# Kernel optimization log

Hardware: AMD Instinct MI355X
Metric: run time of the kernel (lower is better)

Reference implementation:

```python
import jax, jax.numpy as jnp
import numpy as np


def _gru_step(h, x, Wih, Whh, bih, bhh):
    # PyTorch GRU gate order: reset, update, new
    H = h.shape[-1]
    gx = x @ Wih.T + bih            # [B, 3H]
    gh = h @ Whh.T + bhh            # [B, 3H]
    r = jax.nn.sigmoid(gx[:, :H] + gh[:, :H])
    z = jax.nn.sigmoid(gx[:, H:2 * H] + gh[:, H:2 * H])
    n = jnp.tanh(gx[:, 2 * H:] + r * gh[:, 2 * H:])
    return (1.0 - z) * n + z * h


def setup_inputs() -> dict:
    key = jax.random.key(0)
    ks = jax.random.split(key, 20)
    B, S, L = 32, 200, 50
    Vt, Vs = 50000, 30000
    De, Ds, H = 256, 256, 512
    s = 0.05
    f = jnp.float32
    return {
        "method_code": jax.random.randint(ks[0], (B, S), 0, Vt),
        "method_summary": jax.random.randint(ks[1], (B, L), 0, Vs),
        "use_teacher": 1,
        "enc_emb": jax.random.normal(ks[2], (Vt, De), f) * s,
        "enc_Wih": jax.random.normal(ks[3], (3 * H, De), f) * s,
        "enc_Whh": jax.random.normal(ks[4], (3 * H, H), f) * s,
        "enc_bih": jax.random.normal(ks[5], (3 * H,), f) * s,
        "enc_bhh": jax.random.normal(ks[6], (3 * H,), f) * s,
        "dec_emb": jax.random.normal(ks[7], (Vs, Ds), f) * s,
        "dec_Wih": jax.random.normal(ks[8], (3 * H, Ds), f) * s,
        "dec_Whh": jax.random.normal(ks[9], (3 * H, H), f) * s,
        "dec_bih": jax.random.normal(ks[10], (3 * H,), f) * s,
        "dec_bhh": jax.random.normal(ks[11], (3 * H,), f) * s,
        "W1": jax.random.normal(ks[12], (H, 2 * H), f) * s,
        "b1": jax.random.normal(ks[13], (H,), f) * s,
        "W2": jax.random.normal(ks[14], (Vs, H), f) * s,
        "b2": jax.random.normal(ks[15], (Vs,), f) * s,
    }


def reference(method_code, method_summary, use_teacher,
              enc_emb, enc_Wih, enc_Whh, enc_bih, enc_bhh,
              dec_emb, dec_Wih, dec_Whh, dec_bih, dec_bhh,
              W1, b1, W2, b2):
    B = method_code.shape[0]
    H = enc_Whh.shape[1]
    # ---- GRU encoder over code tokens (hidden=None -> zeros) ----
    x_emb = enc_emb[method_code]                       # [B, S, De]
    h0 = jnp.zeros((B, H), x_emb.dtype)

    def enc_step(h, x):
        h = _gru_step(h, x, enc_Wih, enc_Whh, enc_bih, enc_bhh)
        return h, h

    h_last, enc_seq = jax.lax.scan(enc_step, h0, jnp.swapaxes(x_emb, 0, 1))
    enc_out = jnp.swapaxes(enc_seq, 0, 1)              # [B, S, H]

    # ---- attentive GRU decoder, teacher forcing (use_teacher=True) ----
    tokens = method_summary[:, :-1].T                  # [L-1, B]

    def dec_step(h, tok):
        emb = dec_emb[tok]                             # [B, Ds]
        h = _gru_step(h, emb, dec_Wih, dec_Whh, dec_bih, dec_bhh)
        attn = jax.nn.softmax(jnp.einsum('bh,bsh->bs', h, enc_out), axis=-1)
        ctx = jnp.einsum('bs,bsh->bh', attn, enc_out)  # [B, H]
        c = jnp.concatenate([ctx, h], axis=-1)         # [B, 2H]
        out = jax.nn.relu(c @ W1.T + b1) @ W2.T + b2   # [B, Vs]
        return h, out

    _, outs = jax.lax.scan(dec_step, h_last, tokens)   # [L-1, B, Vs]
    return jnp.swapaxes(outs, 0, 1)                    # [B, L-1, Vs]
```

## Files before the change

kernel.cpp:

```cpp
#include <hip/hip_runtime.h>
#include <cmath>

#define WGS  256
#define NWGR 256
#define DOMS 8
#define JGN  32
#define HBDW 2560
#define TDG  4

typedef float    f32x4 __attribute__((ext_vector_type(4)));
typedef unsigned u32x4 __attribute__((ext_vector_type(4)));
typedef short    s16x8 __attribute__((ext_vector_type(8)));
typedef unsigned short u16x4 __attribute__((ext_vector_type(4)));

#define B_   32
#define S_   200
#define L_   50
#define H_   512
#define DE_  256
#define VS_  30000
#define TD_  49
#define G3_  1536

#define OFF_ENC_OUT ((size_t)(S_*B_*G3_) + (size_t)(TD_*B_*G3_))
#define SZ_ENC_OUT  ((size_t)B_*S_*H_)
#define OFF_HBUF    (OFF_ENC_OUT + SZ_ENC_OUT)
#define SZ_HBUF     ((size_t)DOMS*2*HBDW)
#define OFF_CMAT    (OFF_HBUF + SZ_HBUF)
#define SZ_CMAT     ((size_t)TD_*B_*2*H_)
#define OFF_OUT1    (OFF_CMAT + SZ_CMAT)
#define SZ_OUT1     ((size_t)TD_*B_*H_)
#define OFF_W2HI    ((size_t)0)
#define OFF_W2LO    ((size_t)(VS_*H_/2))
#define OFF_O1HI    (OFF_OUT1 + SZ_OUT1)
#define OFF_O1LO    (OFF_O1HI + (size_t)(TD_*B_*H_/2))

#define RSTR 548
#define KBLK 68

__device__ __forceinline__ u32x4 load_u4_cc(const unsigned* p) {
  u32x4 v;
  asm volatile("global_load_dwordx4 %0, %1, off sc0 sc1" : "=v"(v) : "v"(p) : "memory");
  return v;
}

__device__ __forceinline__ float dot4(f32x4 a, f32x4 b) {
  return a.x * b.x + a.y * b.y + a.z * b.z + a.w * b.w;
}

__device__ __forceinline__ unsigned short f2bf(float f) {
  unsigned u = __float_as_uint(f);
  return (unsigned short)((u + 0x7fffu + ((u >> 16) & 1u)) >> 16);
}
__device__ __forceinline__ float bf2f(unsigned short h) {
  return __uint_as_float(((unsigned)h) << 16);
}

__global__ __launch_bounds__(WGS)
void recurrence_kernel(const int* __restrict__ mc, const int* __restrict__ ms,
                       const float* __restrict__ enc_emb,
                       const float* __restrict__ eWih, const float* __restrict__ eBih,
                       const float* __restrict__ dec_emb,
                       const float* __restrict__ dWih, const float* __restrict__ dBih,
                       const float* __restrict__ eWhh, const float* __restrict__ eBhh,
                       const float* __restrict__ dWhh, const float* __restrict__ dBhh,
                       float* __restrict__ enc_out,
                       float* __restrict__ hbuf,
                       float* __restrict__ Cmat)
{
  __shared__ float hlds[4 * RSTR];
  __shared__ float xlds[4 * 256];
  __shared__ float red[768];
  __shared__ float red2[768];

  const int t   = threadIdx.x;
  const int w   = blockIdx.x;
  const int dom = w >> 5;
  const int jg  = w & (JGN - 1);
  const int kh  = t >> 4;
  const int j   = (jg << 4) + (t & 15);
  const int bt_ = t >> 4;
  const int b_g = (dom << 2) + bt_;
  const int xb  = t >> 6, xc = t & 63;
  const int xb_g = (dom << 2) + xb;

  float* hdom = hbuf + (size_t)dom * (2 * HBDW);

  int rr[3], kb[3];
  #pragma unroll
  for (int i = 0; i < 3; ++i) {
    int g = i * 1024 + (t << 2);
    int blk = g / 80;
    rr[i] = g - blk * 80;
    kb[i] = blk << 4;
  }

  f32x4 whh[3][8];
  auto load_whh = [&](const float* __restrict__ W) {
    #pragma unroll
    for (int g = 0; g < 3; ++g)
      #pragma unroll
      for (int c = 0; c < 8; ++c)
        whh[g][c] = *(const f32x4*)(W + (size_t)(g * H_ + j) * H_ + (kh << 5) + (c << 2));
  };
  f32x4 wih[3][4];
  auto load_wih = [&](const float* __restrict__ W) {
    #pragma unroll
    for (int g = 0; g < 3; ++g)
      #pragma unroll
      for (int c = 0; c < 4; ++c)
        wih[g][c] = *(const f32x4*)(W + (size_t)(g * H_ + j) * DE_ + (kh << 4) + (c << 2));
  };
  load_whh(eWhh);
  load_wih(eWih);

  float bhr = 0.f, bhz = 0.f, bhn = 0.f, bxr = 0.f, bxz = 0.f, bxn = 0.f;
  if (t < 64) {
    bhr = eBhh[j]; bhz = eBhh[H_ + j]; bhn = eBhh[2 * H_ + j];
    bxr = eBih[j]; bxz = eBih[H_ + j]; bxn = eBih[2 * H_ + j];
  }

  auto stage_x = [&](int s) {
    const bool enc = (s < S_);
    int tok = enc ? mc[xb_g * S_ + s] : ms[xb_g * L_ + (s - S_)];
    const float* emb = enc ? enc_emb : dec_emb;
    f32x4 xv = *(const f32x4*)(emb + (size_t)tok * DE_ + (xc << 2));
    *(f32x4*)&xlds[xb * 256 + (xc << 2)] = xv;
  };

  auto compute_acx = [&]() {
    float acx[3][4];
    #pragma unroll
    for (int g = 0; g < 3; ++g)
      #pragma unroll
      for (int b = 0; b < 4; ++b) acx[g][b] = 0.f;
    #pragma unroll
    for (int b = 0; b < 4; ++b) {
      const float* xp = &xlds[b * 256 + (kh << 4)];
      #pragma unroll
      for (int c = 0; c < 4; ++c) {
        f32x4 xv = *(const f32x4*)(xp + (c << 2));
        acx[0][b] += dot4(wih[0][c], xv);
        acx[1][b] += dot4(wih[1][c], xv);
        acx[2][b] += dot4(wih[2][c], xv);
      }
    }
    #pragma unroll
    for (int g = 0; g < 3; ++g)
      #pragma unroll
      for (int b = 0; b < 4; ++b) {
        float u = acx[g][b];
        u += __shfl_xor(u, 16); u += __shfl_xor(u, 32);
        acx[g][b] = u;
      }
    if ((t & 48) == 0) {
      const int base = (t >> 6) * 192 + (t & 15) * 12;
      #pragma unroll
      for (int g = 0; g < 3; ++g)
        #pragma unroll
        for (int b = 0; b < 4; ++b)
          red2[base + g * 4 + b] = acx[g][b];
    }
  };

  stage_x(0);
  __syncthreads();
  compute_acx();

  for (int s = 0; s < S_ + TD_; ++s) {
    const bool enc = (s < S_);

    {
      const unsigned* hb = (const unsigned*)(hdom + (size_t)(s & 1) * HBDW);
      const unsigned tagreq = (unsigned)s;
      u32x4 v0, v1, v2;
      while (true) {
        v0 = load_u4_cc(hb + 0 * 1024 + (t << 2));
        v1 = load_u4_cc(hb + 1 * 1024 + (t << 2));
        if (t < 128) v2 = load_u4_cc(hb + 2 * 1024 + (t << 2));
        asm volatile("s_waitcnt vmcnt(0)" ::: "memory");
        bool ok = true;
        if ((rr[0] & 15) == 0) ok &= ((unsigned)v0.x >= tagreq);
        if ((rr[1] & 15) == 0) ok &= ((unsigned)v1.x >= tagreq);
        if (t < 128 && (rr[2] & 15) == 0) ok &= ((unsigned)v2.x >= tagreq);
        if (__all(ok)) break;
        __builtin_amdgcn_s_sleep(1);
      }
      #define SCAT(vv, ii) { \
        _Pragma("unroll") \
        for (int d = 0; d < 4; ++d) { \
          int pos = rr[ii] + d; \
          if ((pos & 15) != 0) { \
            int p = pos - 1 - (pos >> 4); \
            if (p < 64) { \
              int bb = p >> 4, k = kb[ii] + (p & 15); \
              hlds[bb * RSTR + ((k >> 6) * KBLK) + (k & 63)] = __uint_as_float(vv[d]); \
            } } } }
      SCAT(v0, 0) SCAT(v1, 1)
      if (t < 128) { SCAT(v2, 2) }
      #undef SCAT
    }
    __syncthreads();

    {
      float acc[3][4];
      #pragma unroll
      for (int g = 0; g < 3; ++g)
        #pragma unroll
        for (int b = 0; b < 4; ++b) acc[g][b] = 0.f;
      const int hoff = (kh >> 1) * KBLK + (kh & 1) * 32;
      #pragma unroll
      for (int b = 0; b < 4; ++b) {
        const float* hp = &hlds[b * RSTR + hoff];
        #pragma unroll
        for (int c = 0; c < 8; ++c) {
          f32x4 hv = *(const f32x4*)(hp + (c << 2));
          acc[0][b] += dot4(whh[0][c], hv);
          acc[1][b] += dot4(whh[1][c], hv);
          acc[2][b] += dot4(whh[2][c], hv);
        }
      }
      #pragma unroll
      for (int g = 0; g < 3; ++g)
        #pragma unroll
        for (int b = 0; b < 4; ++b) {
          float v = acc[g][b];
          v += __shfl_xor(v, 16); v += __shfl_xor(v, 32);
          acc[g][b] = v;
        }
      if ((t & 48) == 0) {
        const int base = (t >> 6) * 192 + (t & 15) * 12;
        #pragma unroll
        for (int g = 0; g < 3; ++g)
          #pragma unroll
          for (int b = 0; b < 4; ++b)
            red[base + g * 4 + b] = acc[g][b];
      }
    }
    __syncthreads();

    if (s + 1 < S_ + TD_) stage_x(s + 1);

    if (t < 64) {
      float ar = 0.f, az = 0.f, an = 0.f, xr = 0.f, xz = 0.f, xn = 0.f;
      #pragma unroll
      for (int ww = 0; ww < 4; ++ww) {
        const int base = ww * 192 + (t & 15) * 12 + bt_;
        ar += red[base];      az += red[base + 4];  an += red[base + 8];
        xr += red2[base];     xz += red2[base + 4]; xn += red2[base + 8];
      }
      float gxr = xr + bxr, gxz = xz + bxz, gxn = xn + bxn;
      float rg = 1.f / (1.f + expf(-(gxr + ar + bhr)));
      float zg = 1.f / (1.f + expf(-(gxz + az + bhz)));
      float ng = tanhf(gxn + rg * (an + bhn));
      float hprev = hlds[bt_ * RSTR + ((j >> 6) * KBLK) + (j & 63)];
      float hn = (1.f - zg) * ng + zg * hprev;
      if (enc) enc_out[((size_t)b_g * S_ + s) * H_ + j] = hn;
      else     Cmat[((size_t)(s - S_) * B_ + b_g) * (2 * H_) + H_ + j] = hn;

      unsigned* pb = (unsigned*)(hdom + (size_t)((s + 1) & 1) * HBDW) + jg * 80;
      const unsigned tagv = (unsigned)(s + 1);
      float vA = __shfl(hn, (t - 1 - (t >> 4)) & 63);
      unsigned valA = ((t & 15) == 0) ? tagv : __float_as_uint(vA);
      __hip_atomic_store(pb + t, valA, __ATOMIC_RELAXED, __HIP_MEMORY_SCOPE_AGENT);
      float vB = __shfl(hn, (59 + t) & 63);
      if (t < 16) {
        unsigned valB = (t == 0) ? tagv : __float_as_uint(vB);
        __hip_atomic_store(pb + 64 + t, valB, __ATOMIC_RELAXED, __HIP_MEMORY_SCOPE_AGENT);
      }
    }
    __syncthreads();

    if (s + 1 < S_ + TD_) {
      if (s + 1 == S_) {
        load_whh(dWhh);
        load_wih(dWih);
        if (t < 64) {
          bhr = dBhh[j]; bhz = dBhh[H_ + j]; bhn = dBhh[2 * H_ + j];
          bxr = dBih[j]; bxz = dBih[H_ + j]; bxn = dBih[2 * H_ + j];
        }
      }
      compute_acx();
    }
  }
}

__global__ __launch_bounds__(WGS)
void attention_kernel(const float* __restrict__ enc_out,
                      float* __restrict__ Cmat)
{
  const int blk = blockIdx.x;
  const int b = blk / 13, ch = blk % 13;
  const int t = threadIdx.x;
  __shared__ float hlds[TDG][512];
  __shared__ float p[TDG][256];

  for (int idx = t; idx < TDG * 128; idx += WGS) {
    int u = idx >> 7, kq = (idx & 127) << 2;
    int td = ch * TDG + u; if (td >= TD_) td = TD_ - 1;
    *(f32x4*)&hlds[u][kq] =
        *(const f32x4*)(Cmat + ((size_t)td * B_ + b) * (2 * H_) + H_ + kq);
  }
  __syncthreads();

  float sv[TDG] = {0.f, 0.f, 0.f, 0.f};
  if (t < S_) {
    const float* eo = enc_out + ((size_t)b * S_ + t) * H_;
    for (int k = 0; k < H_; k += 4) {
      f32x4 e = *(const f32x4*)(eo + k);
      #pragma unroll
      for (int u = 0; u < TDG; ++u) {
        f32x4 hv = *(const f32x4*)&hlds[u][k];
        sv[u] += e.x * hv.x + e.y * hv.y + e.z * hv.z + e.w * hv.w;
      }
    }
  }
  #pragma unroll
  for (int u = 0; u < TDG; ++u) p[u][t] = (t < S_) ? sv[u] : -1e30f;
  __syncthreads();

  {
    const int wv = t >> 6, l = t & 63;
    float m = fmaxf(fmaxf(p[wv][l], p[wv][l + 64]),
                    fmaxf(p[wv][l + 128], p[wv][l + 192]));
    for (int o = 32; o; o >>= 1) m = fmaxf(m, __shfl_xor(m, o));
    float e0 = expf(p[wv][l] - m),       e1 = expf(p[wv][l + 64] - m);
    float e2 = expf(p[wv][l + 128] - m), e3 = expf(p[wv][l + 192] - m);
    float ssum = (e0 + e1) + (e2 + e3);
    for (int o = 32; o; o >>= 1) ssum += __shfl_xor(ssum, o);
    float inv = 1.f / ssum;
    p[wv][l] = e0 * inv; p[wv][l + 64] = e1 * inv;
    p[wv][l + 128] = e2 * inv; p[wv][l + 192] = e3 * inv;
  }
  __syncthreads();

  float ax[TDG] = {0.f, 0.f, 0.f, 0.f}, ay[TDG] = {0.f, 0.f, 0.f, 0.f};
  const float* eo = enc_out + (size_t)b * S_ * H_ + (t << 1);
  for (int i = 0; i < S_; ++i) {
    float2 v = *(const float2*)(eo + (size_t)i * H_);
    #pragma unroll
    for (int u = 0; u < TDG; ++u) {
      float pi = p[u][i];
      ax[u] += pi * v.x; ay[u] += pi * v.y;
    }
  }
  #pragma unroll
  for (int u = 0; u < TDG; ++u) {
    int td = ch * TDG + u;
    if (td < TD_) {
      float* cd = Cmat + ((size_t)td * B_ + b) * (2 * H_) + (t << 1);
      cd[0] = ax[u]; cd[1] = ay[u];
    }
  }
}

__launch_bounds__(WGS)
__global__ void gemm64_fc1(const float* __restrict__ A,
                           const float* __restrict__ Bw,
                           const float* __restrict__ bias,
                           unsigned short* __restrict__ Ohi,
                           unsigned short* __restrict__ Olo)
{
  const int M = TD_ * B_, N = H_, K = 2 * H_;
  const int BK = 16;
  __shared__ float As[BK][64];
  __shared__ float Bs[BK][64];
  const int m0 = blockIdx.y * 64, n0 = blockIdx.x * 64;
  const int t = threadIdx.x;
  const int tx = t & 15, ty = t >> 4;
  float acc[4][4] = {{0.f}};

  const int row = t >> 2, kk = (t & 3) * 4;
  for (int k0 = 0; k0 < K; k0 += BK) {
    {
      int m = m0 + row;
      f32x4 v = {0.f, 0.f, 0.f, 0.f};
      if (m < M) v = *(const f32x4*)(A + (size_t)m * K + k0 + kk);
      As[kk][row] = v.x; As[kk + 1][row] = v.y; As[kk + 2][row] = v.z; As[kk + 3][row] = v.w;
      int n = n0 + row;
      f32x4 wv = *(const f32x4*)(Bw + (size_t)n * K + k0 + kk);
      Bs[kk][row] = wv.x; Bs[kk + 1][row] = wv.y; Bs[kk + 2][row] = wv.z; Bs[kk + 3][row] = wv.w;
    }
    __syncthreads();
    #pragma unroll
    for (int k = 0; k < BK; ++k) {
      float a[4], bq[4];
      *(f32x4*)a  = *(const f32x4*)&As[k][ty * 4];
      *(f32x4*)bq = *(const f32x4*)&Bs[k][tx * 4];
      #pragma unroll
      for (int i = 0; i < 4; ++i)
        #pragma unroll
        for (int jj = 0; jj < 4; ++jj)
          acc[i][jj] += a[i] * bq[jj];
    }
    __syncthreads();
  }

  #pragma unroll
  for (int i = 0; i < 4; ++i) {
    int m = m0 + ty * 4 + i;
    if (m >= M) continue;
    u16x4 hv, lv;
    #pragma unroll
    for (int jj = 0; jj < 4; ++jj) {
      int n = n0 + tx * 4 + jj;
      float v = fmaxf(acc[i][jj] + bias[n], 0.f);
      unsigned short hb = f2bf(v);
      hv[jj] = hb;
      lv[jj] = f2bf(v - bf2f(hb));
    }
    size_t o = (size_t)m * H_ + n0 + tx * 4;
    *(u16x4*)(Ohi + o) = hv;
    *(u16x4*)(Olo + o) = lv;
  }
}

__global__ __launch_bounds__(WGS)
void cvt_split(const float* __restrict__ x, unsigned short* __restrict__ hi,
               unsigned short* __restrict__ lo, int n4)
{
  int i = blockIdx.x * WGS + threadIdx.x;
  if (i >= n4) return;
  f32x4 v = *(const f32x4*)(x + (size_t)i * 4);
  u16x4 h, l;
  #pragma unroll
  for (int d = 0; d < 4; ++d) {
    unsigned short hb = f2bf(v[d]);
    h[d] = hb;
    l[d] = f2bf(v[d] - bf2f(hb));
  }
  *(u16x4*)(hi + (size_t)i * 4) = h;
  *(u16x4*)(lo + (size_t)i * 4) = l;
}

__global__ __launch_bounds__(WGS, 1)
void gemm_mfma_out(const unsigned short* __restrict__ Ahi,
                   const unsigned short* __restrict__ Alo,
                   const unsigned short* __restrict__ Bhi,
                   const unsigned short* __restrict__ Blo,
                   const float* __restrict__ bias,
                   float* __restrict__ out)
{
  __shared__ char smem[49152];
  const int t = threadIdx.x;
  const int l = t & 63, wv = t >> 6;
  const int r = l & 15, q = l >> 4;
  const int m0 = blockIdx.x * 256;
  const int n0 = blockIdx.y * 128;
  const int M = TD_ * B_, N = VS_, K = H_;
  const int wm = (wv >> 1) * 128;
  const int wn = (wv & 1) * 64;

  int aswz[4]; size_t aoff[4];
  #pragma unroll
  for (int i = 0; i < 4; ++i) {
    int ca = i * 256 + t;
    int row = ca >> 2, cc = ca & 3;
    aswz[i] = row * 64 + ((cc ^ ((row >> 1) & 3)) << 4);
    int gm = m0 + row; if (gm >= M) gm = M - 1;
    aoff[i] = (size_t)gm * K + cc * 8;
  }
  int bswz[2]; size_t boff[2];
  #pragma unroll
  for (int i = 0; i < 2; ++i) {
    int cb = i * 256 + t;
    int row = cb >> 2, cc = cb & 3;
    bswz[i] = row * 64 + ((cc ^ ((row >> 1) & 3)) << 4);
    int gn = n0 + row; if (gn >= N) gn = N - 1;
    boff[i] = (size_t)gn * K + cc * 8;
  }

  u32x4 rg[12];
  auto gload = [&](int k0) {
    #pragma unroll
    for (int i = 0; i < 4; ++i) rg[i]     = *(const u32x4*)(Ahi + aoff[i] + k0);
    #pragma unroll
    for (int i = 0; i < 4; ++i) rg[4 + i] = *(const u32x4*)(Alo + aoff[i] + k0);
    #pragma unroll
    for (int i = 0; i < 2; ++i) rg[8 + i] = *(const u32x4*)(Bhi + boff[i] + k0);
    #pragma unroll
    for (int i = 0; i < 2; ++i) rg[10 + i] = *(const u32x4*)(Blo + boff[i] + k0);
  };
  auto swrite = [&]() {
    #pragma unroll
    for (int i = 0; i < 4; ++i) *(u32x4*)(smem + aswz[i]) = rg[i];
    #pragma unroll
    for (int i = 0; i < 4; ++i) *(u32x4*)(smem + 16384 + aswz[i]) = rg[4 + i];
    #pragma unroll
    for (int i = 0; i < 2; ++i) *(u32x4*)(smem + 32768 + bswz[i]) = rg[8 + i];
    #pragma unroll
    for (int i = 0; i < 2; ++i) *(u32x4*)(smem + 40960 + bswz[i]) = rg[10 + i];
  };

  int afo[8], bfo[4];
  #pragma unroll
  for (int fi = 0; fi < 8; ++fi) {
    int ra = wm + fi * 16 + r;
    afo[fi] = ra * 64 + ((q ^ ((ra >> 1) & 3)) << 4);
  }
  #pragma unroll
  for (int nj = 0; nj < 4; ++nj) {
    int rb = wn + nj * 16 + r;
    bfo[nj] = rb * 64 + ((q ^ ((rb >> 1) & 3)) << 4);
  }

  f32x4 acc[8][4];
  #pragma unroll
  for (int fi = 0; fi < 8; ++fi)
    #pragma unroll
    for (int nj = 0; nj < 4; ++nj) acc[fi][nj] = (f32x4){0.f, 0.f, 0.f, 0.f};

  gload(0);
  swrite();
  __syncthreads();
  const int NS = K / 32;
  for (int s = 0; s < NS; ++s) {
    if (s + 1 < NS) gload((s + 1) * 32);
    s16x8 bh[4], bl[4];
    #pragma unroll
    for (int nj = 0; nj < 4; ++nj) {
      bh[nj] = *(const s16x8*)(smem + 32768 + bfo[nj]);
      bl[nj] = *(const s16x8*)(smem + 40960 + bfo[nj]);
    }
    #pragma unroll
    for (int fi = 0; fi < 8; ++fi) {
      s16x8 ah = *(const s16x8*)(smem + afo[fi]);
      s16x8 al = *(const s16x8*)(smem + 16384 + afo[fi]);
      #pragma unroll
      for (int nj = 0; nj < 4; ++nj) {
        acc[fi][nj] = __builtin_amdgcn_mfma_f32_16x16x32_bf16(ah, bh[nj], acc[fi][nj], 0, 0, 0);
        acc[fi][nj] = __builtin_amdgcn_mfma_f32_16x16x32_bf16(ah, bl[nj], acc[fi][nj], 0, 0, 0);
        acc[fi][nj] = __builtin_amdgcn_mfma_f32_16x16x32_bf16(al, bh[nj], acc[fi][nj], 0, 0, 0);
      }
    }
    __syncthreads();
    if (s + 1 < NS) { swrite(); __syncthreads(); }
  }

  #pragma unroll
  for (int nj = 0; nj < 4; ++nj) {
    int n = n0 + wn + nj * 16 + r;
    if (n >= N) continue;
    float bv = bias[n];
    #pragma unroll
    for (int fi = 0; fi < 8; ++fi) {
      #pragma unroll
      for (int e = 0; e < 4; ++e) {
        int m = m0 + wm + fi * 16 + q * 4 + e;
        if (m < M) {
          int bidx = m & 31, td = m >> 5;
          out[((size_t)bidx * TD_ + td) * (size_t)N + n] = acc[fi][nj][e] + bv;
        }
      }
    }
  }
}

extern "C" void kernel_launch(void* const* d_in, const int* in_sizes, int n_in,
                              void* d_out, int out_size, void* d_ws, size_t ws_size,
                              hipStream_t stream) {
  const int*   method_code    = (const int*)d_in[0];
  const int*   method_summary = (const int*)d_in[1];
  const float* enc_emb = (const float*)d_in[3];
  const float* enc_Wih = (const float*)d_in[4];
  const float* enc_Whh = (const float*)d_in[5];
  const float* enc_bih = (const float*)d_in[6];
  const float* enc_bhh = (const float*)d_in[7];
  const float* dec_emb = (const float*)d_in[8];
  const float* dec_Wih = (const float*)d_in[9];
  const float* dec_Whh = (const float*)d_in[10];
  const float* dec_bih = (const float*)d_in[11];
  const float* dec_bhh = (const float*)d_in[12];
  const float* W1 = (const float*)d_in[13];
  const float* b1 = (const float*)d_in[14];
  const float* W2 = (const float*)d_in[15];
  const float* b2 = (const float*)d_in[16];

  float* ws      = (float*)d_ws;
  float* enc_out = ws + OFF_ENC_OUT;
  float* hbuf    = ws + OFF_HBUF;
  float* Cmat    = ws + OFF_CMAT;
  unsigned short* W2hi = (unsigned short*)(ws + OFF_W2HI);
  unsigned short* W2lo = (unsigned short*)(ws + OFF_W2LO);
  unsigned short* O1hi = (unsigned short*)(ws + OFF_O1HI);
  unsigned short* O1lo = (unsigned short*)(ws + OFF_O1LO);

  hipMemsetAsync(hbuf, 0, SZ_HBUF * sizeof(float), stream);

  dim3 blk(WGS);

  recurrence_kernel<<<NWGR, blk, 0, stream>>>(
      method_code, method_summary,
      enc_emb, enc_Wih, enc_bih,
      dec_emb, dec_Wih, dec_bih,
      enc_Whh, enc_bhh, dec_Whh, dec_bhh,
      enc_out, hbuf, Cmat);

  attention_kernel<<<B_ * 13, blk, 0, stream>>>(enc_out, Cmat);

  cvt_split<<<(VS_ * H_ / 4 + WGS - 1) / WGS, blk, 0, stream>>>(
      W2, W2hi, W2lo, VS_ * H_ / 4);

  gemm64_fc1<<<dim3(H_ / 64, (TD_ * B_ + 63) / 64), blk, 0, stream>>>(
      Cmat, W1, b1, O1hi, O1lo);

  gemm_mfma_out<<<dim3((TD_ * B_ + 255) / 256, (VS_ + 127) / 128), blk, 0, stream>>>(
      O1hi, O1lo, W2hi, W2lo, b2, (float*)d_out);
}
```

Baseline: 1.407 ms.

## Repartition GRU recurrence into 16 batch domains and double-buffer GEMM prefetch

The persistent recurrence kernel now splits the batch into 16 domains of 2 sequences instead of 8 domains of 4. Each workgroup covers 32 hidden units with a 64-wide K slice, so each handoff moves a smaller h buffer and each workgroup does less per-step work, at the cost of more registers for weights and fewer batch rows to reuse them. Separately, the output GEMM prefetches two K-steps ahead using two register buffers, to hide global load latency at the cost of higher register pressure.

Result: no change. 1.395 ms (-0.8%).

```diff
diff --git a/kernel.cpp b/kernel.cpp
--- a/kernel.cpp
+++ b/kernel.cpp
@@ -3,9 +3,9 @@
 
 #define WGS  256
 #define NWGR 256
-#define DOMS 8
-#define JGN  32
-#define HBDW 2560
+#define DOMS 16
+#define JGN  16
+#define HBDW 1280
 #define TDG  4
 
 typedef float    f32x4 __attribute__((ext_vector_type(4)));
@@ -56,7 +56,7 @@
   return __uint_as_float(((unsigned)h) << 16);
 }
 
-__global__ __launch_bounds__(WGS)
+__global__ __launch_bounds__(WGS, 1)
 void recurrence_kernel(const int* __restrict__ mc, const int* __restrict__ ms,
                        const float* __restrict__ enc_emb,
                        const float* __restrict__ eWih, const float* __restrict__ eBih,
@@ -68,48 +68,44 @@
                        float* __restrict__ hbuf,
                        float* __restrict__ Cmat)
 {
-  __shared__ float hlds[4 * RSTR];
-  __shared__ float xlds[4 * 256];
+  __shared__ float hlds[2 * RSTR];
+  __shared__ float xlds[2 * 256];
   __shared__ float red[768];
   __shared__ float red2[768];
 
   const int t   = threadIdx.x;
   const int w   = blockIdx.x;
-  const int dom = w >> 5;
+  const int dom = w >> 4;
   const int jg  = w & (JGN - 1);
-  const int kh  = t >> 4;
-  const int j   = (jg << 4) + (t & 15);
-  const int bt_ = t >> 4;
-  const int b_g = (dom << 2) + bt_;
+  const int jl  = t & 31;
+  const int kh  = t >> 5;
+  const int j   = (jg << 5) + jl;
+  const int bt_ = t >> 5;
+  const int b_g = (dom << 1) + bt_;
   const int xb  = t >> 6, xc = t & 63;
-  const int xb_g = (dom << 2) + xb;
+  const int xb_g = (dom << 1) + xb;
 
   float* hdom = hbuf + (size_t)dom * (2 * HBDW);
 
-  int rr[3], kb[3];
-  #pragma unroll
-  for (int i = 0; i < 3; ++i) {
-    int g = i * 1024 + (t << 2);
-    int blk = g / 80;
-    rr[i] = g - blk * 80;
-    kb[i] = blk << 4;
-  }
-
-  f32x4 whh[3][8];
+  int rr0, kb0, rr1, kb1;
+  { int g = t << 2; int blk = g / 80; rr0 = g - blk * 80; kb0 = blk << 5; }
+  { int g = 1024 + (t << 2); int blk = g / 80; rr1 = g - blk * 80; kb1 = blk << 5; }
+
+  f32x4 whh[3][16];
   auto load_whh = [&](const float* __restrict__ W) {
     #pragma unroll
     for (int g = 0; g < 3; ++g)
       #pragma unroll
+      for (int c = 0; c < 16; ++c)
+        whh[g][c] = *(const f32x4*)(W + (size_t)(g * H_ + j) * H_ + (kh << 6) + (c << 2));
+  };
+  f32x4 wih[3][8];
+  auto load_wih = [&](const float* __restrict__ W) {
+    #pragma unroll
+    for (int g = 0; g < 3; ++g)
+      #pragma unroll
       for (int c = 0; c < 8; ++c)
-        whh[g][c] = *(const f32x4*)(W + (size_t)(g * H_ + j) * H_ + (kh << 5) + (c << 2));
-  };
-  f32x4 wih[3][4];
-  auto load_wih = [&](const float* __restrict__ W) {
-    #pragma unroll
-    for (int g = 0; g < 3; ++g)
-      #pragma unroll
-      for (int c = 0; c < 4; ++c)
-        wih[g][c] = *(const f32x4*)(W + (size_t)(g * H_ + j) * DE_ + (kh << 4) + (c << 2));
+        wih[g][c] = *(const f32x4*)(W + (size_t)(g * H_ + j) * DE_ + (kh << 5) + (c << 2));
   };
   load_whh(eWhh);
   load_wih(eWih);
@@ -121,24 +117,24 @@
   }
 
   auto stage_x = [&](int s) {
-    const bool enc = (s < S_);
-    int tok = enc ? mc[xb_g * S_ + s] : ms[xb_g * L_ + (s - S_)];
-    const float* emb = enc ? enc_emb : dec_emb;
-    f32x4 xv = *(const f32x4*)(emb + (size_t)tok * DE_ + (xc << 2));
-    *(f32x4*)&xlds[xb * 256 + (xc << 2)] = xv;
+    if (t < 128) {
+      const bool enc = (s < S_);
+      int tok = enc ? mc[xb_g * S_ + s] : ms[xb_g * L_ + (s - S_)];
+      const float* emb = enc ? enc_emb : dec_emb;
+      f32x4 xv = *(const f32x4*)(emb + (size_t)tok * DE_ + (xc << 2));
+      *(f32x4*)&xlds[xb * 256 + (xc << 2)] = xv;
+    }
   };
 
   auto compute_acx = [&]() {
-    float acx[3][4];
-    #pragma unroll
-    for (int g = 0; g < 3; ++g)
-      #pragma unroll
-      for (int b = 0; b < 4; ++b) acx[g][b] = 0.f;
-    #pragma unroll
-    for (int b = 0; b < 4; ++b) {
-      const float* xp = &xlds[b * 256 + (kh << 4)];
-      #pragma unroll
-      for (int c = 0; c < 4; ++c) {
+    float acx[3][2];
+    #pragma unroll
+    for (int g = 0; g < 3; ++g) { acx[g][0] = 0.f; acx[g][1] = 0.f; }
+    #pragma unroll
+    for (int b = 0; b < 2; ++b) {
+      const float* xp = &xlds[b * 256 + (kh << 5)];
+      #pragma unroll
+      for (int c = 0; c < 8; ++c) {
         f32x4 xv = *(const f32x4*)(xp + (c << 2));
         acx[0][b] += dot4(wih[0][c], xv);
         acx[1][b] += dot4(wih[1][c], xv);
@@ -148,18 +144,18 @@
     #pragma unroll
     for (int g = 0; g < 3; ++g)
       #pragma unroll
-      for (int b = 0; b < 4; ++b) {
+      for (int b = 0; b < 2; ++b) {
         float u = acx[g][b];
-        u += __shfl_xor(u, 16); u += __shfl_xor(u, 32);
+        u += __shfl_xor(u, 32);
         acx[g][b] = u;
       }
-    if ((t & 48) == 0) {
-      const int base = (t >> 6) * 192 + (t & 15) * 12;
-      #pragma unroll
-      for (int g = 0; g < 3; ++g)
-        #pragma unroll
-        for (int b = 0; b < 4; ++b)
-          red2[base + g * 4 + b] = acx[g][b];
+    if ((t & 32) == 0) {
+      const int base = (t >> 6) * 192 + (t & 31) * 6;
+      #pragma unroll
+      for (int g = 0; g < 3; ++g) {
+        red2[base + g * 2 + 0] = acx[g][0];
+        red2[base + g * 2 + 1] = acx[g][1];
+      }
     }
   };
 
@@ -173,47 +169,42 @@
     {
       const unsigned* hb = (const unsigned*)(hdom + (size_t)(s & 1) * HBDW);
       const unsigned tagreq = (unsigned)s;
-      u32x4 v0, v1, v2;
+      u32x4 v0, v1;
       while (true) {
-        v0 = load_u4_cc(hb + 0 * 1024 + (t << 2));
-        v1 = load_u4_cc(hb + 1 * 1024 + (t << 2));
-        if (t < 128) v2 = load_u4_cc(hb + 2 * 1024 + (t << 2));
+        v0 = load_u4_cc(hb + (t << 2));
+        if (t < 64) v1 = load_u4_cc(hb + 1024 + (t << 2));
         asm volatile("s_waitcnt vmcnt(0)" ::: "memory");
         bool ok = true;
-        if ((rr[0] & 15) == 0) ok &= ((unsigned)v0.x >= tagreq);
-        if ((rr[1] & 15) == 0) ok &= ((unsigned)v1.x >= tagreq);
-        if (t < 128 && (rr[2] & 15) == 0) ok &= ((unsigned)v2.x >= tagreq);
+        if ((rr0 & 15) == 0) ok &= ((unsigned)v0.x >= tagreq);
+        if (t < 64 && (rr1 & 15) == 0) ok &= ((unsigned)v1.x >= tagreq);
         if (__all(ok)) break;
         __builtin_amdgcn_s_sleep(1);
       }
-      #define SCAT(vv, ii) { \
+      #define SCAT(vv, rrX, kbX) { \
         _Pragma("unroll") \
         for (int d = 0; d < 4; ++d) { \
-          int pos = rr[ii] + d; \
+          int pos = rrX + d; \
           if ((pos & 15) != 0) { \
             int p = pos - 1 - (pos >> 4); \
             if (p < 64) { \
-              int bb = p >> 4, k = kb[ii] + (p & 15); \
+              int bb = p >> 5, k = kbX + (p & 31); \
               hlds[bb * RSTR + ((k >> 6) * KBLK) + (k & 63)] = __uint_as_float(vv[d]); \
             } } } }
-      SCAT(v0, 0) SCAT(v1, 1)
-      if (t < 128) { SCAT(v2, 2) }
+      SCAT(v0, rr0, kb0)
+      if (t < 64) { SCAT(v1, rr1, kb1) }
       #undef SCAT
     }
     __syncthreads();
 
     {
-      float acc[3][4];
-      #pragma unroll
-      for (int g = 0; g < 3; ++g)
+      float acc[3][2];
+      #pragma unroll
+      for (int g = 0; g < 3; ++g) { acc[g][0] = 0.f; acc[g][1] = 0.f; }
+      #pragma unroll
+      for (int b = 0; b < 2; ++b) {
+        const float* hp = &hlds[b * RSTR + kh * KBLK];
         #pragma unroll
-        for (int b = 0; b < 4; ++b) acc[g][b] = 0.f;
-      const int hoff = (kh >> 1) * KBLK + (kh & 1) * 32;
-      #pragma unroll
-      for (int b = 0; b < 4; ++b) {
-        const float* hp = &hlds[b * RSTR + hoff];
-        #pragma unroll
-        for (int c = 0; c < 8; ++c) {
+        for (int c = 0; c < 16; ++c) {
           f32x4 hv = *(const f32x4*)(hp + (c << 2));
           acc[0][b] += dot4(whh[0][c], hv);
           acc[1][b] += dot4(whh[1][c], hv);
@@ -223,18 +214,18 @@
       #pragma unroll
       for (int g = 0; g < 3; ++g)
         #pragma unroll
-        for (int b = 0; b < 4; ++b) {
+        for (int b = 0; b < 2; ++b) {
           float v = acc[g][b];
-          v += __shfl_xor(v, 16); v += __shfl_xor(v, 32);
+          v += __shfl_xor(v, 32);
           acc[g][b] = v;
         }
-      if ((t & 48) == 0) {
-        const int base = (t >> 6) * 192 + (t & 15) * 12;
+      if ((t & 32) == 0) {
+        const int base = (t >> 6) * 192 + (t & 31) * 6;
         #pragma unroll
-        for (int g = 0; g < 3; ++g)
-          #pragma unroll
-          for (int b = 0; b < 4; ++b)
-            red[base + g * 4 + b] = acc[g][b];
+        for (int g = 0; g < 3; ++g) {
+          red[base + g * 2 + 0] = acc[g][0];
+          red[base + g * 2 + 1] = acc[g][1];
+        }
       }
     }
     __syncthreads();
@@ -242,13 +233,13 @@
     if (s + 1 < S_ + TD_) stage_x(s + 1);
 
     if (t < 64) {
-      float ar = 0.f, az = 0.f, an = 0.f, xr = 0.f, xz = 0.f, xn = 0.f;
-      #pragma unroll
-      for (int ww = 0; ww < 4; ++ww) {
-        const int base = ww * 192 + (t & 15) * 12 + bt_;
-        ar += red[base];      az += red[base + 4];  an += red[base + 8];
-        xr += red2[base];     xz += red2[base + 4]; xn += red2[base + 8];
-      }
+      const int base0 = (t & 31) * 6 + bt_;
+      float ar = red[base0] + red[192 + base0] + red[384 + base0] + red[576 + base0];
+      float az = red[base0 + 2] + red[192 + base0 + 2] + red[384 + base0 + 2] + red[576 + base0 + 2];
+      float an = red[base0 + 4] + red[192 + base0 + 4] + red[384 + base0 + 4] + red[576 + base0 + 4];
+      float xr = red2[base0] + red2[192 + base0] + red2[384 + base0] + red2[576 + base0];
+      float xz = red2[base0 + 2] + red2[192 + base0 + 2] + red2[384 + base0 + 2] + red2[576 + base0 + 2];
+      float xn = red2[base0 + 4] + red2[192 + base0 + 4] + red2[384 + base0 + 4] + red2[576 + base0 + 4];
       float gxr = xr + bxr, gxz = xz + bxz, gxn = xn + bxn;
       float rg = 1.f / (1.f + expf(-(gxr + ar + bhr)));
       float zg = 1.f / (1.f + expf(-(gxz + az + bhz)));
@@ -470,27 +461,25 @@
     boff[i] = (size_t)gn * K + cc * 8;
   }
 
-  u32x4 rg[12];
-  auto gload = [&](int k0) {
-    #pragma unroll
-    for (int i = 0; i < 4; ++i) rg[i]     = *(const u32x4*)(Ahi + aoff[i] + k0);
-    #pragma unroll
-    for (int i = 0; i < 4; ++i) rg[4 + i] = *(const u32x4*)(Alo + aoff[i] + k0);
-    #pragma unroll
-    for (int i = 0; i < 2; ++i) rg[8 + i] = *(const u32x4*)(Bhi + boff[i] + k0);
-    #pragma unroll
-    for (int i = 0; i < 2; ++i) rg[10 + i] = *(const u32x4*)(Blo + boff[i] + k0);
-  };
-  auto swrite = [&]() {
-    #pragma unroll
-    for (int i = 0; i < 4; ++i) *(u32x4*)(smem + aswz[i]) = rg[i];
-    #pragma unroll
-    for (int i = 0; i < 4; ++i) *(u32x4*)(smem + 16384 + aswz[i]) = rg[4 + i];
-    #pragma unroll
-    for (int i = 0; i < 2; ++i) *(u32x4*)(smem + 32768 + bswz[i]) = rg[8 + i];
-    #pragma unroll
-    for (int i = 0; i < 2; ++i) *(u32x4*)(smem + 40960 + bswz[i]) = rg[10 + i];
-  };
+  u32x4 rgA[12], rgB[12];
+  #define GLOAD(rg, k0) { \
+    _Pragma("unroll") \
+    for (int i = 0; i < 4; ++i) rg[i]     = *(const u32x4*)(Ahi + aoff[i] + (k0)); \
+    _Pragma("unroll") \
+    for (int i = 0; i < 4; ++i) rg[4 + i] = *(const u32x4*)(Alo + aoff[i] + (k0)); \
+    _Pragma("unroll") \
+    for (int i = 0; i < 2; ++i) rg[8 + i] = *(const u32x4*)(Bhi + boff[i] + (k0)); \
+    _Pragma("unroll") \
+    for (int i = 0; i < 2; ++i) rg[10 + i] = *(const u32x4*)(Blo + boff[i] + (k0)); }
+  #define SWRITE(rg) { \
+    _Pragma("unroll") \
+    for (int i = 0; i < 4; ++i) *(u32x4*)(smem + aswz[i]) = rg[i]; \
+    _Pragma("unroll") \
+    for (int i = 0; i < 4; ++i) *(u32x4*)(smem + 16384 + aswz[i]) = rg[4 + i]; \
+    _Pragma("unroll") \
+    for (int i = 0; i < 2; ++i) *(u32x4*)(smem + 32768 + bswz[i]) = rg[8 + i]; \
+    _Pragma("unroll") \
+    for (int i = 0; i < 2; ++i) *(u32x4*)(smem + 40960 + bswz[i]) = rg[10 + i]; }
 
   int afo[8], bfo[4];
   #pragma unroll
@@ -510,12 +499,13 @@
     #pragma unroll
     for (int nj = 0; nj < 4; ++nj) acc[fi][nj] = (f32x4){0.f, 0.f, 0.f, 0.f};
 
-  gload(0);
-  swrite();
+  GLOAD(rgA, 0)
+  SWRITE(rgA)
+  GLOAD(rgA, 32)
+  GLOAD(rgB, 64)
   __syncthreads();
   const int NS = K / 32;
   for (int s = 0; s < NS; ++s) {
-    if (s + 1 < NS) gload((s + 1) * 32);
     s16x8 bh[4], bl[4];
     #pragma unroll
     for (int nj = 0; nj < 4; ++nj) {
@@ -534,8 +524,16 @@
       }
     }
     __syncthreads();
-    if (s + 1 < NS) { swrite(); __syncthreads(); }
-  }
+    if (s + 1 < NS) {
+      if (s & 1) { SWRITE(rgB) } else { SWRITE(rgA) }
+      __syncthreads();
+      if (s + 3 < NS) {
+        if (s & 1) { GLOAD(rgB, (s + 3) * 32) } else { GLOAD(rgA, (s + 3) * 32) }
+      }
+    }
+  }
+  #undef GLOAD
+  #undef SWRITE
 
   #pragma unroll
   for (int nj = 0; nj < 4; ++nj) {
```
